# Performance work log

Hardware: AMD Instinct MI355X
Metric: run time of the kernel (lower is better)

Reference implementation:

```python
import jax, jax.numpy as jnp
import numpy as np

N, D, M, E = 8192, 2048, 512, 4
SCALE = 1.0

def setup_inputs() -> dict:
    key = jax.random.key(0)
    ks = jax.random.split(key, 6)
    x = jax.random.normal(ks[0], (N, D), dtype=jnp.float32)
    domains = jax.random.randint(ks[1], (N,), 0, E, dtype=jnp.int64)
    # torch Linear default init ~ U(-1/sqrt(fan_in), 1/sqrt(fan_in)); use scaled normals
    W1 = jax.random.normal(ks[2], (E, M, D), dtype=jnp.float32) / np.sqrt(D)
    b1 = jax.random.normal(ks[3], (E, M), dtype=jnp.float32) * 0.01
    W2 = jax.random.normal(ks[4], (E, D, M), dtype=jnp.float32) / np.sqrt(M)
    b2 = jax.random.normal(ks[5], (E, D), dtype=jnp.float32) * 0.01
    return {"x": x, "domains": domains, "W1": W1, "b1": b1, "W2": W2, "b2": b2}

def reference(x, domains, W1, b1, W2, b2):
    # Each expert: Linear(D->M) -> ReLU -> Linear(M->D); token n uses expert domains[n].
    # Dense compute over all experts, then per-token select via one-hot (jit-friendly
    # equivalent of the boolean-mask gather/scatter in the torch code).
    h = jax.nn.relu(jnp.einsum('nd,emd->enm', x, W1) + b1[:, None, :])   # [E,N,M]
    y = jnp.einsum('enm,edm->end', h, W2) + b2[:, None, :]               # [E,N,D]
    sel = jax.nn.one_hot(domains, E, dtype=x.dtype)                       # [N,E]
    out = x + SCALE * jnp.einsum('end,ne->nd', y, sel)
    return out
```

## Files before the change

kernel.cpp:

```cpp
#include <hip/hip_runtime.h>
#include <hip/hip_bf16.h>
#include <cstdint>
#include <type_traits>

#define N_TOK 8192
#define DDIM  2048
#define MDIM  512
#define NEXP  4
#define PADROWS (N_TOK + NEXP * 256)

typedef __bf16 bf16x4 __attribute__((ext_vector_type(4)));
typedef __bf16 bf16x8 __attribute__((ext_vector_type(8)));
typedef float  f32x4  __attribute__((ext_vector_type(4)));

__device__ int g_counts[NEXP];
__device__ int g_idx[NEXP * N_TOK];
__device__ __align__(16) __hip_bfloat16 g_Xp[(size_t)(DDIM / 64) * PADROWS * 64];
__device__ __align__(16) __hip_bfloat16 g_Hp[(size_t)(MDIM / 64) * PADROWS * 64];
__device__ __align__(16) __hip_bfloat16 g_W1t[(size_t)NEXP * MDIM * DDIM];
__device__ __align__(16) __hip_bfloat16 g_W2t[(size_t)NEXP * DDIM * MDIM];

__global__ void zero_counts_kernel() {
    if (threadIdx.x < NEXP) g_counts[threadIdx.x] = 0;
}

__global__ void bucket_kernel(const void* __restrict__ domv) {
    const int i    = blockIdx.x * blockDim.x + threadIdx.x;
    const int lane = threadIdx.x & 63;

    const long long* d64 = (const long long*)domv;
    long long probe = d64[lane];
    bool mode64 = (__ballot(probe >= 0 && probe < NEXP) == ~0ull);

    const int e = mode64 ? (int)d64[i] : ((const int*)domv)[i];

#pragma unroll
    for (int ex = 0; ex < NEXP; ++ex) {
        unsigned long long m = __ballot(e == ex);
        if (m == 0) continue;
        int cnt    = __popcll(m);
        int leader = __ffsll((long long)m) - 1;
        int base   = 0;
        if (lane == leader) base = atomicAdd(&g_counts[ex], cnt);
        base = __shfl(base, leader);
        if (e == ex) {
            int prefix = __popcll(m & ((1ull << lane) - 1ull));
            g_idx[ex * N_TOK + base + prefix] = i;
        }
    }
}

__global__ __launch_bounds__(256)
void cvt_w_kernel(const float* __restrict__ w1, const float* __restrict__ w2) {
    const bool is1 = (blockIdx.y == 0);
    const float* src = is1 ? w1 : w2;
    __hip_bfloat16* dst = is1 ? g_W1t : g_W2t;
    const int total8 = NEXP * MDIM * DDIM / 8;
    const int stride = gridDim.x * blockDim.x;
    for (int g8 = blockIdx.x * blockDim.x + threadIdx.x; g8 < total8; g8 += stride) {
        const int e   = g8 >> 17;
        const int rem = g8 & 131071;
        int row, kt, within;
        if (is1) { row = rem >> 8; int d0 = (rem & 255) * 8; kt = d0 >> 6; within = d0 & 63; }
        else     { row = rem >> 6; int m0 = (rem & 63) * 8;  kt = m0 >> 6; within = m0 & 63; }
        const float* s = src + (size_t)g8 * 8;
        f32x4 a = *(const f32x4*)s;
        f32x4 b = *(const f32x4*)(s + 4);
        bf16x8 r;
        r[0] = (__bf16)a[0]; r[1] = (__bf16)a[1]; r[2] = (__bf16)a[2]; r[3] = (__bf16)a[3];
        r[4] = (__bf16)b[0]; r[5] = (__bf16)b[1]; r[6] = (__bf16)b[2]; r[7] = (__bf16)b[3];
        const size_t d = is1 ? (((size_t)(e * 32 + kt) * MDIM + row) * 64 + within)
                             : (((size_t)(e * 8 + kt) * DDIM + row) * 64 + within);
        *(bf16x8*)&dst[d] = r;
    }
}

__global__ __launch_bounds__(256)
void cvt_xp_kernel(const float* __restrict__ x) {
    int c[NEXP], off[NEXP + 1]; off[0] = 0;
#pragma unroll
    for (int e = 0; e < NEXP; ++e) { c[e] = g_counts[e]; off[e + 1] = off[e] + ((c[e] + 255) & ~255); }

    const int gs = blockIdx.x;
    int e = 0;
#pragma unroll
    for (int t = 0; t < NEXP - 1; ++t) if (gs >= off[t + 1]) e = t + 1;
    if (gs >= off[e + 1]) return;
    int ls = gs - off[e];
    if (ls >= c[e]) ls = c[e] - 1;
    const int tok = g_idx[e * N_TOK + ls];

    const int d0 = threadIdx.x * 8;
    const float* s = x + (size_t)tok * DDIM + d0;
    f32x4 a = *(const f32x4*)s;
    f32x4 b = *(const f32x4*)(s + 4);
    bf16x8 r;
    r[0] = (__bf16)a[0]; r[1] = (__bf16)a[1]; r[2] = (__bf16)a[2]; r[3] = (__bf16)a[3];
    r[4] = (__bf16)b[0]; r[5] = (__bf16)b[1]; r[6] = (__bf16)b[2]; r[7] = (__bf16)b[3];
    *(bf16x8*)&g_Xp[((size_t)(d0 >> 6) * PADROWS + gs) * 64 + (d0 & 63)] = r;
}

__device__ __forceinline__ void gl16(const __hip_bfloat16* g, __hip_bfloat16* l) {
    __builtin_amdgcn_global_load_lds(
        (const __attribute__((address_space(1))) void*)g,
        (__attribute__((address_space(3))) void*)l,
        16, 0, 0);
}

template <int N>
__device__ __forceinline__ void wait_vm() {
    if constexpr (N == 0)      asm volatile("s_waitcnt vmcnt(0)" ::: "memory");
    else if constexpr (N == 6) asm volatile("s_waitcnt vmcnt(6)" ::: "memory");
    else if constexpr (N == 8) asm volatile("s_waitcnt vmcnt(8)" ::: "memory");
    else                       asm volatile("s_waitcnt vmcnt(0)" ::: "memory");
}

template <int BN, int KDIM, int NCOLS, bool RELU, bool TILEOUT, typename TC>
__device__ __forceinline__ void gemm_core(const __hip_bfloat16* __restrict__ A,
                                          const __hip_bfloat16* __restrict__ B,
                                          const float* __restrict__ bias,
                                          const float* __restrict__ resid,
                                          TC* __restrict__ C) {
    constexpr int BM    = 128;
    constexpr int BK    = 64;
    constexpr int KTS   = KDIM / BK;
    constexpr int NACH  = 4;
    constexpr int NBCH  = BN / 32;
    constexpr int LPS   = NACH + NBCH;
    constexpr int NJ    = BN / 32;
    constexpr int NSTEP = KTS;

    const int rt = blockIdx.x;
    const int ct = blockIdx.y;

    int cv[NEXP], off[NEXP + 1]; off[0] = 0;
#pragma unroll
    for (int x = 0; x < NEXP; ++x) { cv[x] = g_counts[x]; off[x + 1] = off[x] + ((cv[x] + 255) & ~255); }
    const int r0 = rt * BM;
    if (r0 >= off[NEXP]) return;
    int e = 0;
#pragma unroll
    for (int t = 0; t < NEXP - 1; ++t) if (r0 >= off[t + 1]) e = t + 1;

    __shared__ __align__(16) __hip_bfloat16 sA[2][BM * BK];
    __shared__ __align__(16) __hip_bfloat16 sB[2][BN * BK];
    __shared__ int sTok[BM];

    const int tid  = threadIdx.x;
    const int wave = tid >> 6;
    const int lane = tid & 63;

    if (!TILEOUT) {
        if (tid < BM) {
            int ls = r0 + tid - off[e];
            sTok[tid] = (ls < cv[e]) ? g_idx[e * N_TOK + ls] : -1;
        }
        __syncthreads();
    }

    const int srow = wave * 8 + (lane >> 3);
    const int ssl  = ((lane & 7) ^ (lane >> 3)) * 8;

    auto stage = [&](int buf, int kt) {
#pragma unroll
        for (int q = 0; q < NACH; ++q)
            gl16(A + ((size_t)kt * PADROWS + r0 + q * 32 + srow) * 64 + ssl,
                 &sA[buf][(q * 256 + wave * 64) * 8]);
#pragma unroll
        for (int q = 0; q < NBCH; ++q)
            gl16(B + ((size_t)(e * KTS + kt) * NCOLS + ct * BN + q * 32 + srow) * 64 + ssl,
                 &sB[buf][(q * 256 + wave * 64) * 8]);
    };

    const int wm   = (wave >> 1) * 64;
    const int wn   = (wave & 1) * (BN / 2);
    const int frow = lane & 15;
    int cof[2];
#pragma unroll
    for (int ks = 0; ks < 2; ++ks)
        cof[ks] = ((ks * 4 + (lane >> 4)) ^ (lane & 7)) * 8;

    f32x4 acc[4][NJ] = {};

    auto compute = [&](int buf) {
        const __hip_bfloat16* pA = &sA[buf][0];
        const __hip_bfloat16* pB = &sB[buf][0];
#pragma unroll
        for (int ks = 0; ks < 2; ++ks) {
            bf16x8 bfr[NJ];
#pragma unroll
            for (int j = 0; j < NJ; ++j)
                bfr[j] = *(const bf16x8*)&pB[(wn + j * 16 + frow) * BK + cof[ks]];
#pragma unroll
            for (int i = 0; i < 4; ++i) {
                bf16x8 af = *(const bf16x8*)&pA[(wm + i * 16 + frow) * BK + cof[ks]];
#pragma unroll
                for (int j = 0; j < NJ; ++j)
                    acc[i][j] = __builtin_amdgcn_mfma_f32_16x16x32_bf16(
                        bfr[j], af, acc[i][j], 0, 0, 0);
            }
        }
    };

    stage(0, 0);
    stage(1, 1);

    int cur = 0;
    for (int t = 0; t < NSTEP - 1; ++t) {
        wait_vm<LPS>();
        __builtin_amdgcn_s_barrier();
        __builtin_amdgcn_sched_barrier(0);
        compute(cur);
        asm volatile("" ::: "memory");
        __builtin_amdgcn_s_barrier();
        if (t + 2 < NSTEP) stage(cur, t + 2);
        cur ^= 1;
    }
    wait_vm<0>();
    __builtin_amdgcn_s_barrier();
    __builtin_amdgcn_sched_barrier(0);
    compute(cur);

    const int lrow = lane & 15;
    const int lcol = (lane >> 4) * 4;
#pragma unroll
    for (int i = 0; i < 4; ++i) {
        const int rl = wm + i * 16 + lrow;
        const int gs = r0 + rl;
#pragma unroll
        for (int j = 0; j < NJ; ++j) {
            const int col = ct * BN + wn + j * 16 + lcol;
            const f32x4 bv = *(const f32x4*)&bias[(size_t)e * NCOLS + col];
            f32x4 v = acc[i][j] + bv;
            if (RELU) {
#pragma unroll
                for (int r = 0; r < 4; ++r) v[r] = fmaxf(v[r], 0.0f);
            }
            if constexpr (TILEOUT) {
                bf16x4 h;
                h[0] = (__bf16)v[0]; h[1] = (__bf16)v[1];
                h[2] = (__bf16)v[2]; h[3] = (__bf16)v[3];
                *(bf16x4*)&C[((size_t)(col >> 6) * PADROWS + gs) * 64 + (col & 63)] = h;
            } else {
                const int tk = sTok[rl];
                if (tk >= 0) {
                    v += *(const f32x4*)&resid[(size_t)tk * NCOLS + col];
                    *(f32x4*)&C[(size_t)tk * NCOLS + col] = v;
                }
            }
        }
    }
}

__global__ __launch_bounds__(256)
void gemm1_kernel(const float* __restrict__ b1) {
    gemm_core<64, DDIM, MDIM, true, true, __hip_bfloat16>(
        g_Xp, g_W1t, b1, nullptr, g_Hp);
}

__global__ __launch_bounds__(256)
void gemm2_kernel(const float* __restrict__ x,
                  const float* __restrict__ b2,
                  float* __restrict__ out) {
    gemm_core<128, MDIM, DDIM, false, false, float>(
        g_Hp, g_W2t, b2, x, out);
}

extern "C" void kernel_launch(void* const* d_in, const int* in_sizes, int n_in,
                              void* d_out, int out_size, void* d_ws, size_t ws_size,
                              hipStream_t stream) {
    const float* x  = (const float*)d_in[0];
    const void*  dm = d_in[1];
    const float* W1 = (const float*)d_in[2];
    const float* b1 = (const float*)d_in[3];
    const float* W2 = (const float*)d_in[4];
    const float* b2 = (const float*)d_in[5];
    float* out = (float*)d_out;

    zero_counts_kernel<<<1, 64, 0, stream>>>();
    bucket_kernel<<<N_TOK / 256, 256, 0, stream>>>(dm);
    cvt_w_kernel<<<dim3(1024, 2), 256, 0, stream>>>(W1, W2);
    cvt_xp_kernel<<<PADROWS, 256, 0, stream>>>(x);

    gemm1_kernel<<<dim3(PADROWS / 128, MDIM / 64), 256, 0, stream>>>(b1);
    gemm2_kernel<<<dim3(PADROWS / 128, DDIM / 128), 256, 0, stream>>>(x, b2, out);
}
```

Measured before the change: 241.8 us.

## Merge bucketing and conversion launches, widen GEMM1 column tile

Replaces the counter-zeroing kernel and the atomic-based bucket kernel with one 1024-thread block. That block counts tokens per expert and builds the index lists with a shared-memory prefix scan, so the order is deterministic. The activation gather/convert and the weight conversion now run in a single kernel launch split by blockIdx.y. GEMM1 uses a 128-wide column tile instead of 64. The pipeline drops from six launches to four, which cuts launch overhead and atomics, but GEMM1 gets half as many blocks and the serial single-block scan could become a small bottleneck.

```diff
diff --git a/kernel.cpp b/kernel.cpp
--- a/kernel.cpp
+++ b/kernel.cpp
@@ -15,49 +15,97 @@
 
 __device__ int g_counts[NEXP];
 __device__ int g_idx[NEXP * N_TOK];
-__device__ __align__(16) __hip_bfloat16 g_Xp[(size_t)(DDIM / 64) * PADROWS * 64];
-__device__ __align__(16) __hip_bfloat16 g_Hp[(size_t)(MDIM / 64) * PADROWS * 64];
+__device__ __align__(16) __hip_bfloat16 g_Xp[(size_t)DDIM * PADROWS];
+__device__ __align__(16) __hip_bfloat16 g_Hp[(size_t)MDIM * PADROWS];
 __device__ __align__(16) __hip_bfloat16 g_W1t[(size_t)NEXP * MDIM * DDIM];
 __device__ __align__(16) __hip_bfloat16 g_W2t[(size_t)NEXP * DDIM * MDIM];
 
-__global__ void zero_counts_kernel() {
-    if (threadIdx.x < NEXP) g_counts[threadIdx.x] = 0;
-}
-
-__global__ void bucket_kernel(const void* __restrict__ domv) {
-    const int i    = blockIdx.x * blockDim.x + threadIdx.x;
-    const int lane = threadIdx.x & 63;
+__global__ __launch_bounds__(1024)
+void bucket1_kernel(const void* __restrict__ domv) {
+    __shared__ int sc[NEXP][1024];
+    const int tid  = threadIdx.x;
+    const int lane = tid & 63;
 
     const long long* d64 = (const long long*)domv;
     long long probe = d64[lane];
     bool mode64 = (__ballot(probe >= 0 && probe < NEXP) == ~0ull);
 
-    const int e = mode64 ? (int)d64[i] : ((const int*)domv)[i];
-
-#pragma unroll
-    for (int ex = 0; ex < NEXP; ++ex) {
-        unsigned long long m = __ballot(e == ex);
-        if (m == 0) continue;
-        int cnt    = __popcll(m);
-        int leader = __ffsll((long long)m) - 1;
-        int base   = 0;
-        if (lane == leader) base = atomicAdd(&g_counts[ex], cnt);
-        base = __shfl(base, leader);
-        if (e == ex) {
-            int prefix = __popcll(m & ((1ull << lane) - 1ull));
-            g_idx[ex * N_TOK + base + prefix] = i;
-        }
-    }
+    int e[8];
+    int cnt[NEXP] = {};
+#pragma unroll
+    for (int k = 0; k < 8; ++k) {
+        const int i = tid * 8 + k;
+        e[k] = mode64 ? (int)d64[i] : ((const int*)domv)[i];
+#pragma unroll
+        for (int x = 0; x < NEXP; ++x) cnt[x] += (e[k] == x);
+    }
+#pragma unroll
+    for (int x = 0; x < NEXP; ++x) sc[x][tid] = cnt[x];
+    __syncthreads();
+
+    for (int o = 1; o < 1024; o <<= 1) {
+        int v[NEXP];
+        if (tid >= o) {
+#pragma unroll
+            for (int x = 0; x < NEXP; ++x) v[x] = sc[x][tid - o];
+        }
+        __syncthreads();
+        if (tid >= o) {
+#pragma unroll
+            for (int x = 0; x < NEXP; ++x) sc[x][tid] += v[x];
+        }
+        __syncthreads();
+    }
+
+    int base[NEXP];
+#pragma unroll
+    for (int x = 0; x < NEXP; ++x) base[x] = sc[x][tid] - cnt[x];
+#pragma unroll
+    for (int k = 0; k < 8; ++k) {
+#pragma unroll
+        for (int x = 0; x < NEXP; ++x) {
+            if (e[k] == x) g_idx[x * N_TOK + base[x]] = tid * 8 + k;
+            base[x] += (e[k] == x);
+        }
+    }
+    if (tid < NEXP) g_counts[tid] = sc[tid][1023];
 }
 
 __global__ __launch_bounds__(256)
-void cvt_w_kernel(const float* __restrict__ w1, const float* __restrict__ w2) {
-    const bool is1 = (blockIdx.y == 0);
-    const float* src = is1 ? w1 : w2;
-    __hip_bfloat16* dst = is1 ? g_W1t : g_W2t;
-    const int total8 = NEXP * MDIM * DDIM / 8;
-    const int stride = gridDim.x * blockDim.x;
-    for (int g8 = blockIdx.x * blockDim.x + threadIdx.x; g8 < total8; g8 += stride) {
+void cvt_all_kernel(const float* __restrict__ x,
+                    const float* __restrict__ w1,
+                    const float* __restrict__ w2) {
+    if (blockIdx.y == 0) {
+        int c[NEXP], off[NEXP + 1]; off[0] = 0;
+#pragma unroll
+        for (int e = 0; e < NEXP; ++e) { c[e] = g_counts[e]; off[e + 1] = off[e] + ((c[e] + 255) & ~255); }
+        const int gs = blockIdx.x;
+        int e = 0;
+#pragma unroll
+        for (int t = 0; t < NEXP - 1; ++t) if (gs >= off[t + 1]) e = t + 1;
+        if (gs >= off[e + 1]) return;
+        int ls = gs - off[e];
+        if (ls >= c[e]) ls = c[e] - 1;
+        if (ls < 0) ls = 0;
+        const int tok = g_idx[e * N_TOK + ls];
+
+        const int d0 = threadIdx.x * 8;
+        const float* s = x + (size_t)tok * DDIM + d0;
+        f32x4 a = *(const f32x4*)s;
+        f32x4 b = *(const f32x4*)(s + 4);
+        bf16x8 r;
+        r[0] = (__bf16)a[0]; r[1] = (__bf16)a[1]; r[2] = (__bf16)a[2]; r[3] = (__bf16)a[3];
+        r[4] = (__bf16)b[0]; r[5] = (__bf16)b[1]; r[6] = (__bf16)b[2]; r[7] = (__bf16)b[3];
+        *(bf16x8*)&g_Xp[((size_t)(d0 >> 6) * PADROWS + gs) * 64 + (d0 & 63)] = r;
+    } else {
+        constexpr int HALF = NEXP * MDIM * DDIM / 8;
+        const int gtid = blockIdx.x * 256 + threadIdx.x;
+        if (gtid >= 2 * HALF) return;
+        const bool is1 = (gtid < HALF);
+        const int g8 = is1 ? gtid : gtid - HALF;
+        const float* src = is1 ? w1 : w2;
+        __hip_bfloat16* dst = is1 ? g_W1t : g_W2t;
+
         const int e   = g8 >> 17;
         const int rem = g8 & 131071;
         int row, kt, within;
@@ -75,31 +123,6 @@
     }
 }
 
-__global__ __launch_bounds__(256)
-void cvt_xp_kernel(const float* __restrict__ x) {
-    int c[NEXP], off[NEXP + 1]; off[0] = 0;
-#pragma unroll
-    for (int e = 0; e < NEXP; ++e) { c[e] = g_counts[e]; off[e + 1] = off[e] + ((c[e] + 255) & ~255); }
-
-    const int gs = blockIdx.x;
-    int e = 0;
-#pragma unroll
-    for (int t = 0; t < NEXP - 1; ++t) if (gs >= off[t + 1]) e = t + 1;
-    if (gs >= off[e + 1]) return;
-    int ls = gs - off[e];
-    if (ls >= c[e]) ls = c[e] - 1;
-    const int tok = g_idx[e * N_TOK + ls];
-
-    const int d0 = threadIdx.x * 8;
-    const float* s = x + (size_t)tok * DDIM + d0;
-    f32x4 a = *(const f32x4*)s;
-    f32x4 b = *(const f32x4*)(s + 4);
-    bf16x8 r;
-    r[0] = (__bf16)a[0]; r[1] = (__bf16)a[1]; r[2] = (__bf16)a[2]; r[3] = (__bf16)a[3];
-    r[4] = (__bf16)b[0]; r[5] = (__bf16)b[1]; r[6] = (__bf16)b[2]; r[7] = (__bf16)b[3];
-    *(bf16x8*)&g_Xp[((size_t)(d0 >> 6) * PADROWS + gs) * 64 + (d0 & 63)] = r;
-}
-
 __device__ __forceinline__ void gl16(const __hip_bfloat16* g, __hip_bfloat16* l) {
     __builtin_amdgcn_global_load_lds(
         (const __attribute__((address_space(1))) void*)g,
@@ -110,9 +133,7 @@
 template <int N>
 __device__ __forceinline__ void wait_vm() {
     if constexpr (N == 0)      asm volatile("s_waitcnt vmcnt(0)" ::: "memory");
-    else if constexpr (N == 6) asm volatile("s_waitcnt vmcnt(6)" ::: "memory");
     else if constexpr (N == 8) asm volatile("s_waitcnt vmcnt(8)" ::: "memory");
-    else                       asm volatile("s_waitcnt vmcnt(0)" ::: "memory");
 }
 
 template <int BN, int KDIM, int NCOLS, bool RELU, bool TILEOUT, typename TC>
@@ -123,12 +144,12 @@
                                           TC* __restrict__ C) {
     constexpr int BM    = 128;
     constexpr int BK    = 64;
-    constexpr int KTS   = KDIM / BK;
+    constexpr int KT    = KDIM / BK;
     constexpr int NACH  = 4;
     constexpr int NBCH  = BN / 32;
     constexpr int LPS   = NACH + NBCH;
     constexpr int NJ    = BN / 32;
-    constexpr int NSTEP = KTS;
+    constexpr int NSTEP = KT;
 
     const int rt = blockIdx.x;
     const int ct = blockIdx.y;
@@ -168,7 +189,7 @@
                  &sA[buf][(q * 256 + wave * 64) * 8]);
 #pragma unroll
         for (int q = 0; q < NBCH; ++q)
-            gl16(B + ((size_t)(e * KTS + kt) * NCOLS + ct * BN + q * 32 + srow) * 64 + ssl,
+            gl16(B + ((size_t)(e * KT + kt) * NCOLS + ct * BN + q * 32 + srow) * 64 + ssl,
                  &sB[buf][(q * 256 + wave * 64) * 8]);
     };
 
@@ -254,7 +275,7 @@
 
 __global__ __launch_bounds__(256)
 void gemm1_kernel(const float* __restrict__ b1) {
-    gemm_core<64, DDIM, MDIM, true, true, __hip_bfloat16>(
+    gemm_core<128, DDIM, MDIM, true, true, __hip_bfloat16>(
         g_Xp, g_W1t, b1, nullptr, g_Hp);
 }
 
@@ -277,11 +298,8 @@
     const float* b2 = (const float*)d_in[5];
     float* out = (float*)d_out;
 
-    zero_counts_kernel<<<1, 64, 0, stream>>>();
-    bucket_kernel<<<N_TOK / 256, 256, 0, stream>>>(dm);
-    cvt_w_kernel<<<dim3(1024, 2), 256, 0, stream>>>(W1, W2);
-    cvt_xp_kernel<<<PADROWS, 256, 0, stream>>>(x);
-
-    gemm1_kernel<<<dim3(PADROWS / 128, MDIM / 64), 256, 0, stream>>>(b1);
+    bucket1_kernel<<<1, 1024, 0, stream>>>(dm);
+    cvt_all_kernel<<<dim3(PADROWS, 2), 256, 0, stream>>>(x, W1, W2);
+    gemm1_kernel<<<dim3(PADROWS / 128, MDIM / 128), 256, 0, stream>>>(b1);
     gemm2_kernel<<<dim3(PADROWS / 128, DDIM / 128), 256, 0, stream>>>(x, b2, out);
 }
```

New measurement: 240.3 us. Within noise of the previous version (-0.6%).
